# Kernel tuning notes

Hardware: AMD Instinct MI355X
Metric: run time of the kernel (lower is better)

The kernel has to match this reference:

```python
import jax, jax.numpy as jnp
import numpy as np

H = 4096
I = 11008
S = 4096
B = 1


def _swiglu_mlp(x, Wgu, Wd):
    # x: [B, T, H]; Wgu: [H, 2I]; Wd: [I, H]
    gu = jnp.einsum('bth,hi->bti', x, Wgu)
    gate, up = gu[..., :I], gu[..., I:]
    return jnp.einsum('bti,ih->bth', jax.nn.silu(gate) * up, Wd)


def setup_inputs() -> dict:
    key = jax.random.key(0)
    ks = jax.random.split(key, 5)
    scale_h = 1.0 / np.sqrt(H)
    scale_i = 1.0 / np.sqrt(I)
    hidden_states = jax.random.normal(ks[0], (B, S, H), dtype=jnp.float32)
    lang_ids = jnp.arange(S // 2, dtype=jnp.int64 if jax.config.jax_enable_x64 else jnp.int32)
    vision_ids = jnp.arange(S // 2, S, dtype=lang_ids.dtype)
    Wgu_lang = jax.random.normal(ks[1], (H, 2 * I), dtype=jnp.float32) * scale_h
    Wd_lang = jax.random.normal(ks[2], (I, H), dtype=jnp.float32) * scale_i
    Wgu_vis = jax.random.normal(ks[3], (H, 2 * I), dtype=jnp.float32) * scale_h
    Wd_vis = jax.random.normal(ks[4], (I, H), dtype=jnp.float32) * scale_i
    return {
        'hidden_states': hidden_states,
        'lang_ids': lang_ids,
        'vision_ids': vision_ids,
        'Wgu_lang': Wgu_lang,
        'Wd_lang': Wd_lang,
        'Wgu_vis': Wgu_vis,
        'Wd_vis': Wd_vis,
    }


def reference(hidden_states, lang_ids, vision_ids, Wgu_lang, Wd_lang, Wgu_vis, Wd_vis):
    # gather-by-token-type -> SwiGLU MLP per expert -> scatter-combine
    lang_out = _swiglu_mlp(hidden_states[:, lang_ids], Wgu_lang, Wd_lang)
    vis_out = _swiglu_mlp(hidden_states[:, vision_ids], Wgu_vis, Wd_vis)
    out = jnp.zeros_like(hidden_states)
    out = out.at[:, lang_ids].set(lang_out)
    out = out.at[:, vision_ids].set(vis_out)
    return out
```

## Files before the change

kernel.cpp:

```cpp
#include <hip/hip_runtime.h>
#include <hip/hip_bf16.h>


#define HDIM 4096
#define IDIM 11008
#define N2   22016
#define MTOK 2048
#define BM   128
#define BN   128
#define BK   64
#define KT1  64
#define KT2  172
#define NB1  86
#define NB2  32

typedef unsigned short ushort_t;
using f32x4  = __attribute__((ext_vector_type(4))) float;
using bf16x8 = __attribute__((ext_vector_type(8))) short;
using u32x2  = __attribute__((ext_vector_type(2))) unsigned int;
using u32x4  = __attribute__((ext_vector_type(4))) unsigned int;

__device__ __forceinline__ unsigned int bf16rne(float f) {
    unsigned int u = __builtin_bit_cast(unsigned int, f);
    return (u + 0x7FFFu + ((u >> 16) & 1u)) >> 16;
}
__device__ __forceinline__ unsigned int pack2(float lo, float hi) {
    return bf16rne(lo) | (bf16rne(hi) << 16);
}
__device__ __forceinline__ void gl_lds16(const void* g, void* l) {
    __builtin_amdgcn_global_load_lds(
        (const __attribute__((address_space(1))) void*)g,
        (__attribute__((address_space(3))) void*)l, 16, 0, 0);
}


__global__ __launch_bounds__(256)
void conv_x(const float* __restrict__ X, ushort_t* __restrict__ XP) {
    int bid = blockIdx.x;
    int rb = bid >> 6, kt = bid & 63;
    int t = threadIdx.x;
    int r0 = t >> 4, c4 = t & 15;
    ushort_t* tp = XP + (long)bid * 8192;
#pragma unroll
    for (int p = 0; p < 8; ++p) {
        int r = r0 + p * 16;
        f32x4 v = *(const f32x4*)(X + (long)(rb * 128 + r) * HDIM + kt * 64 + c4 * 4);
        u32x2 pk = { pack2(v[0], v[1]), pack2(v[2], v[3]) };
        int off = r * 64 + ((((c4 >> 1) ^ (r & 7)) << 3)) + ((c4 & 1) << 2);
        *(u32x2*)&tp[off] = pk;
    }
}

__device__ __forceinline__ void conv_w_tile(const float* W, ushort_t* tp, long ld,
                                            long krow0, long col0, int t) {
    int kp = t >> 5, c4 = t & 31;
    const float* p = W + (krow0 + kp * 8) * ld + col0 + c4 * 4;
    f32x4 v[8];
#pragma unroll
    for (int j = 0; j < 8; ++j) v[j] = *(const f32x4*)(p + (long)j * ld);
#pragma unroll
    for (int c = 0; c < 4; ++c) {
        int n = c4 * 4 + c;
        u32x4 pk = { pack2(v[0][c], v[1][c]), pack2(v[2][c], v[3][c]),
                     pack2(v[4][c], v[5][c]), pack2(v[6][c], v[7][c]) };
        int off = n * 64 + ((kp ^ (n & 7)) << 3);
        *(u32x4*)&tp[off] = pk;
    }
}

__global__ __launch_bounds__(256)
void conv_wgu(const float* __restrict__ W, ushort_t* __restrict__ WP) {
    int bid = blockIdx.x;
    int e = bid & 1, kt = (bid >> 1) & 63, nb = bid >> 7;
    conv_w_tile(W, WP + (long)bid * 8192, N2, (long)kt * 64,
                (long)e * IDIM + (long)nb * 128, threadIdx.x);
}

__global__ __launch_bounds__(256)
void conv_wd(const float* __restrict__ W, ushort_t* __restrict__ WP) {
    int bid = blockIdx.x;
    int kt = bid % KT2, nb = bid / KT2;
    conv_w_tile(W, WP + (long)bid * 8192, HDIM, (long)kt * 64,
                (long)nb * 128, threadIdx.x);
}

__global__ __launch_bounds__(256, 2)
void gu2_kernel(const ushort_t* __restrict__ XP, const ushort_t* __restrict__ WP,
                ushort_t* __restrict__ HP) {
    __shared__ ushort_t lds[24576];

    int nwg = gridDim.x;
    int cpx = nwg >> 3;
    int sw  = (blockIdx.x & 7) * cpx + (blockIdx.x >> 3);
    int mblk = sw & 15;
    int nblk = sw >> 4;

    const int t    = threadIdx.x;
    const int lane = t & 63;
    const int w    = t >> 6;
    const int wm   = w >> 1, wn = w & 1;
    const int rr   = lane & 15, g4 = lane >> 4;

    f32x4 accg[4][4] = {};
    f32x4 accu[4][4] = {};

    const ushort_t* srcA0 = XP + (long)(mblk * 64) * 8192;
    const ushort_t* srcG0 = WP + (long)(nblk * 64) * 2 * 8192;

    for (int kt = 0; kt < KT1; ++kt) {
        __syncthreads();
        const ushort_t* sA = srcA0 + (long)kt * 8192;
        const ushort_t* sG = srcG0 + (long)kt * 2 * 8192;
#pragma unroll
        for (int j = 0; j < 12; ++j) {
            int q = j * 4 + w;
            const ushort_t* s = (j < 4) ? sA : (j < 8) ? sG : (sG + 8192);
            gl_lds16(s + ((q & 15) << 9) + lane * 8, &lds[q << 9]);
        }
        __syncthreads();
#pragma unroll
        for (int ks = 0; ks < 2; ++ks) {
            const int c = ks * 4 + g4;
            bf16x8 a[4], bg[4], bu[4];
#pragma unroll
            for (int mf = 0; mf < 4; ++mf) {
                int r = wm * 64 + mf * 16 + rr;
                a[mf] = *(const bf16x8*)&lds[r * 64 + ((c ^ (r & 7)) << 3)];
            }
#pragma unroll
            for (int nf = 0; nf < 4; ++nf) {
                int r = wn * 64 + nf * 16 + rr;
                int off = r * 64 + ((c ^ (r & 7)) << 3);
                bg[nf] = *(const bf16x8*)&lds[8192 + off];
                bu[nf] = *(const bf16x8*)&lds[16384 + off];
            }
#pragma unroll
            for (int mf = 0; mf < 4; ++mf)
#pragma unroll
                for (int nf = 0; nf < 4; ++nf) {
                    accg[mf][nf] = __builtin_amdgcn_mfma_f32_16x16x32_bf16(a[mf], bg[nf], accg[mf][nf], 0, 0, 0);
                    accu[mf][nf] = __builtin_amdgcn_mfma_f32_16x16x32_bf16(a[mf], bu[nf], accu[mf][nf], 0, 0, 0);
                }
        }
    }
#pragma unroll
    for (int nf = 0; nf < 4; ++nf) {
        int nloc = wn * 64 + nf * 16 + rr;
        int kt2  = nblk * 2 + (nloc >> 6);
        int kk   = nloc & 63;
        ushort_t* tp = HP + (long)(mblk * KT2 + kt2) * 8192;
        int obase = ((kk >> 3) << 3) + (kk & 7);
#pragma unroll
        for (int mf = 0; mf < 4; ++mf)
#pragma unroll
            for (int i = 0; i < 4; ++i) {
                int r = wm * 64 + mf * 16 + g4 * 4 + i;
                float gv = accg[mf][nf][i];
                float uv = accu[mf][nf][i];
                float s  = gv / (1.0f + __expf(-gv));
                int off = r * 64 + ((((kk >> 3) ^ (r & 7)) << 3)) + (kk & 7);
                tp[off] = (ushort_t)bf16rne(s * uv);
            }
        (void)obase;
    }
}

__global__ __launch_bounds__(256, 3)
void down2_kernel(const ushort_t* __restrict__ HP, const ushort_t* __restrict__ WP,
                  float* __restrict__ Out) {
    __shared__ ushort_t lds[16384];

    int nwg = gridDim.x;
    int cpx = nwg >> 3;
    int sw  = (blockIdx.x & 7) * cpx + (blockIdx.x >> 3);
    int mblk = sw & 15;
    int nblk = sw >> 4;

    const int t    = threadIdx.x;
    const int lane = t & 63;
    const int w    = t >> 6;
    const int wm   = w >> 1, wn = w & 1;
    const int rr   = lane & 15, g4 = lane >> 4;

    f32x4 acc[4][4] = {};

    const ushort_t* srcA0 = HP + (long)(mblk * KT2) * 8192;
    const ushort_t* srcB0 = WP + (long)(nblk * KT2) * 8192;

    for (int kt = 0; kt < KT2; ++kt) {
        __syncthreads();
        const ushort_t* sA = srcA0 + (long)kt * 8192;
        const ushort_t* sB = srcB0 + (long)kt * 8192;
#pragma unroll
        for (int j = 0; j < 8; ++j) {
            int q = j * 4 + w;
            const ushort_t* s = (j < 4) ? sA : sB;
            gl_lds16(s + ((q & 15) << 9) + lane * 8, &lds[q << 9]);
        }
        __syncthreads();
#pragma unroll
        for (int ks = 0; ks < 2; ++ks) {
            const int c = ks * 4 + g4;
            bf16x8 a[4], b[4];
#pragma unroll
            for (int mf = 0; mf < 4; ++mf) {
                int r = wm * 64 + mf * 16 + rr;
                a[mf] = *(const bf16x8*)&lds[r * 64 + ((c ^ (r & 7)) << 3)];
            }
#pragma unroll
            for (int nf = 0; nf < 4; ++nf) {
                int r = wn * 64 + nf * 16 + rr;
                b[nf] = *(const bf16x8*)&lds[8192 + r * 64 + ((c ^ (r & 7)) << 3)];
            }
#pragma unroll
            for (int mf = 0; mf < 4; ++mf)
#pragma unroll
                for (int nf = 0; nf < 4; ++nf)
                    acc[mf][nf] = __builtin_amdgcn_mfma_f32_16x16x32_bf16(a[mf], b[nf], acc[mf][nf], 0, 0, 0);
        }
    }
#pragma unroll
    for (int mf = 0; mf < 4; ++mf)
#pragma unroll
        for (int nf = 0; nf < 4; ++nf)
#pragma unroll
            for (int i = 0; i < 4; ++i) {
                int m = mblk * 128 + wm * 64 + mf * 16 + g4 * 4 + i;
                int n = nblk * 128 + wn * 64 + nf * 16 + rr;
                Out[(long)m * HDIM + n] = acc[mf][nf][i];
            }
}

__device__ __forceinline__ int swz(int r) { return ((r >> 2) + ((r & 3) << 1)) & 7; }

__global__ __launch_bounds__(256, 2)
void gu_kernel(const float* __restrict__ X, const float* __restrict__ W,
               ushort_t* __restrict__ Hbuf) {
    __shared__ short As[BM * BK];
    __shared__ short Bg[BN * BK];
    __shared__ short Bu[BN * BK];
    int nwg = gridDim.x;
    int cpx = nwg >> 3;
    int sw  = (blockIdx.x & 7) * cpx + (blockIdx.x >> 3);
    int mblk = sw & 15, nblk = sw >> 4;
    const int m0 = mblk * BM, n0 = nblk * BN;
    const int t = threadIdx.x, lane = t & 63, w = t >> 6;
    const int wm = w >> 1, wn = w & 1, rr = lane & 15, g4 = lane >> 4;
    const int nc = t & 31, kc = t >> 5;
    f32x4 accg[4][4] = {}, accu[4][4] = {};
    for (int k0 = 0; k0 < HDIM; k0 += BK) {
        __syncthreads();
#pragma unroll
        for (int i = 0; i < 8; ++i) {
            int idx = t + i * 256, m = idx >> 4, c4 = idx & 15;
            f32x4 v = *(const f32x4*)(X + (long)(m0 + m) * HDIM + k0 + c4 * 4);
            u32x2 pk = { pack2(v[0], v[1]), pack2(v[2], v[3]) };
            *(u32x2*)&As[(m << 6) + ((((c4 >> 1) + swz(m)) & 7) << 3) + ((c4 & 1) << 2)] = pk;
        }
#pragma unroll
        for (int e = 0; e < 2; ++e) {
            const float* Wp = W + (long)(k0 + kc * 8) * N2 + (e ? (IDIM + n0) : n0) + nc * 4;
            short* Bl = e ? Bu : Bg;
#pragma unroll
            for (int h = 0; h < 2; ++h) {
                f32x4 r0 = *(const f32x4*)(Wp + (long)(h * 4 + 0) * N2);
                f32x4 r1 = *(const f32x4*)(Wp + (long)(h * 4 + 1) * N2);
                f32x4 r2 = *(const f32x4*)(Wp + (long)(h * 4 + 2) * N2);
                f32x4 r3 = *(const f32x4*)(Wp + (long)(h * 4 + 3) * N2);
#pragma unroll
                for (int c2 = 0; c2 < 4; ++c2) {
                    int n = nc * 4 + c2;
                    u32x2 pk = { pack2(r0[c2], r1[c2]), pack2(r2[c2], r3[c2]) };
                    *(u32x2*)&Bl[(n << 6) + (((kc + swz(n)) & 7) << 3) + (h << 2)] = pk;
                }
            }
        }
        __syncthreads();
#pragma unroll
        for (int ks = 0; ks < 2; ++ks) {
            bf16x8 a[4], bg[4], bu[4];
#pragma unroll
            for (int mf = 0; mf < 4; ++mf) {
                int r = wm * 64 + mf * 16 + rr;
                a[mf] = *(const bf16x8*)&As[(r << 6) + ((((ks * 4 + g4) + swz(r)) & 7) << 3)];
            }
#pragma unroll
            for (int nf = 0; nf < 4; ++nf) {
                int r = wn * 64 + nf * 16 + rr;
                int off = (r << 6) + ((((ks * 4 + g4) + swz(r)) & 7) << 3);
                bg[nf] = *(const bf16x8*)&Bg[off];
                bu[nf] = *(const bf16x8*)&Bu[off];
            }
#pragma unroll
            for (int mf = 0; mf < 4; ++mf)
#pragma unroll
                for (int nf = 0; nf < 4; ++nf) {
                    accg[mf][nf] = __builtin_amdgcn_mfma_f32_16x16x32_bf16(a[mf], bg[nf], accg[mf][nf], 0, 0, 0);
                    accu[mf][nf] = __builtin_amdgcn_mfma_f32_16x16x32_bf16(a[mf], bu[nf], accu[mf][nf], 0, 0, 0);
                }
        }
    }
#pragma unroll
    for (int mf = 0; mf < 4; ++mf)
#pragma unroll
        for (int nf = 0; nf < 4; ++nf)
#pragma unroll
            for (int i = 0; i < 4; ++i) {
                int m = m0 + wm * 64 + mf * 16 + g4 * 4 + i;
                int n = n0 + wn * 64 + nf * 16 + rr;
                float gv = accg[mf][nf][i], uv = accu[mf][nf][i];
                Hbuf[(long)m * IDIM + n] = (ushort_t)bf16rne(gv / (1.0f + __expf(-gv)) * uv);
            }
}

__global__ __launch_bounds__(256, 2)
void down_kernel(const ushort_t* __restrict__ Hbuf, const float* __restrict__ W,
                 float* __restrict__ Out) {
    __shared__ short As[BM * BK];
    __shared__ short Bs[BN * BK];
    int nwg = gridDim.x;
    int cpx = nwg >> 3;
    int sw  = (blockIdx.x & 7) * cpx + (blockIdx.x >> 3);
    int mblk = sw & 15, nblk = sw >> 4;
    const int m0 = mblk * BM, n0 = nblk * BN;
    const int t = threadIdx.x, lane = t & 63, w = t >> 6;
    const int wm = w >> 1, wn = w & 1, rr = lane & 15, g4 = lane >> 4;
    const int nc = t & 31, kc = t >> 5;
    f32x4 acc[4][4] = {};
    for (int k0 = 0; k0 < IDIM; k0 += BK) {
        __syncthreads();
#pragma unroll
        for (int i = 0; i < 4; ++i) {
            int idx = t + i * 256, m = idx >> 3, kc8 = idx & 7;
            u32x4 v = *(const u32x4*)(Hbuf + (long)(m0 + m) * IDIM + k0 + kc8 * 8);
            *(u32x4*)&As[(m << 6) + (((kc8 + swz(m)) & 7) << 3)] = v;
        }
        {
            const float* Wp = W + (long)(k0 + kc * 8) * HDIM + n0 + nc * 4;
#pragma unroll
            for (int h = 0; h < 2; ++h) {
                f32x4 r0 = *(const f32x4*)(Wp + (long)(h * 4 + 0) * HDIM);
                f32x4 r1 = *(const f32x4*)(Wp + (long)(h * 4 + 1) * HDIM);
                f32x4 r2 = *(const f32x4*)(Wp + (long)(h * 4 + 2) * HDIM);
                f32x4 r3 = *(const f32x4*)(Wp + (long)(h * 4 + 3) * HDIM);
#pragma unroll
                for (int c2 = 0; c2 < 4; ++c2) {
                    int n = nc * 4 + c2;
                    u32x2 pk = { pack2(r0[c2], r1[c2]), pack2(r2[c2], r3[c2]) };
                    *(u32x2*)&Bs[(n << 6) + (((kc + swz(n)) & 7) << 3) + (h << 2)] = pk;
                }
            }
        }
        __syncthreads();
#pragma unroll
        for (int ks = 0; ks < 2; ++ks) {
            bf16x8 a[4], b[4];
#pragma unroll
            for (int mf = 0; mf < 4; ++mf) {
                int r = wm * 64 + mf * 16 + rr;
                a[mf] = *(const bf16x8*)&As[(r << 6) + ((((ks * 4 + g4) + swz(r)) & 7) << 3)];
            }
#pragma unroll
            for (int nf = 0; nf < 4; ++nf) {
                int r = wn * 64 + nf * 16 + rr;
                b[nf] = *(const bf16x8*)&Bs[(r << 6) + ((((ks * 4 + g4) + swz(r)) & 7) << 3)];
            }
#pragma unroll
            for (int mf = 0; mf < 4; ++mf)
#pragma unroll
                for (int nf = 0; nf < 4; ++nf)
                    acc[mf][nf] = __builtin_amdgcn_mfma_f32_16x16x32_bf16(a[mf], b[nf], acc[mf][nf], 0, 0, 0);
        }
    }
#pragma unroll
    for (int mf = 0; mf < 4; ++mf)
#pragma unroll
        for (int nf = 0; nf < 4; ++nf)
#pragma unroll
            for (int i = 0; i < 4; ++i) {
                int m = m0 + wm * 64 + mf * 16 + g4 * 4 + i;
                int n = n0 + wn * 64 + nf * 16 + rr;
                Out[(long)m * HDIM + n] = acc[mf][nf][i];
            }
}

extern "C" void kernel_launch(void* const* d_in, const int* in_sizes, int n_in,
                              void* d_out, int out_size, void* d_ws, size_t ws_size,
                              hipStream_t stream) {
    const float* x     = (const float*)d_in[0];
    const float* Wgu_l = (const float*)d_in[3];
    const float* Wd_l  = (const float*)d_in[4];
    const float* Wgu_v = (const float*)d_in[5];
    const float* Wd_v  = (const float*)d_in[6];
    float* out         = (float*)d_out;

    const size_t XP_B = (size_t)16 * KT1 * 16384;
    const size_t HP_B = (size_t)16 * KT2 * 16384;
    const size_t WP_B = (size_t)NB1 * KT1 * 2 * 16384;
    const size_t NEED = XP_B + HP_B + WP_B;

    if (ws_size >= NEED) {
        ushort_t* XP = (ushort_t*)d_ws;
        ushort_t* HP = XP + XP_B / 2;
        ushort_t* WP = HP + HP_B / 2;
        for (int e = 0; e < 2; ++e) {
            const float* xe = x + (long)e * MTOK * HDIM;
            float*       oe = out + (long)e * MTOK * HDIM;
            conv_x  <<<dim3(16 * KT1),      dim3(256), 0, stream>>>(xe, XP);
            conv_wgu<<<dim3(NB1 * KT1 * 2), dim3(256), 0, stream>>>(e ? Wgu_v : Wgu_l, WP);
            gu2_kernel<<<dim3(16 * NB1),    dim3(256), 0, stream>>>(XP, WP, HP);
            conv_wd <<<dim3(NB2 * KT2),     dim3(256), 0, stream>>>(e ? Wd_v : Wd_l, WP);
            down2_kernel<<<dim3(16 * NB2),  dim3(256), 0, stream>>>(HP, WP, oe);
        }
    } else {
        ushort_t* hbuf = (ushort_t*)d_ws;
        for (int e = 0; e < 2; ++e) {
            const float* Wgu = e ? Wgu_v : Wgu_l;
            const float* Wd  = e ? Wd_v  : Wd_l;
            const float* xe  = x   + (long)e * MTOK * HDIM;
            float*       oe  = out + (long)e * MTOK * HDIM;
            gu_kernel  <<<dim3(16 * NB1), dim3(256), 0, stream>>>(xe, Wgu, hbuf);
            down_kernel<<<dim3(16 * NB2), dim3(256), 0, stream>>>(hbuf, Wd, oe);
        }
    }
}
```

Before: 1.469 ms.

## Double-buffer LDS with 256-row tiles and 8 waves in both GEMM kernels

```diff
diff --git a/kernel.cpp b/kernel.cpp
--- a/kernel.cpp
+++ b/kernel.cpp
@@ -37,34 +37,19 @@
 __global__ __launch_bounds__(256)
 void conv_x(const float* __restrict__ X, ushort_t* __restrict__ XP) {
     int bid = blockIdx.x;
-    int rb = bid >> 6, kt = bid & 63;
+    int mb = bid >> 6, kt = bid & 63;
     int t = threadIdx.x;
     int r0 = t >> 4, c4 = t & 15;
-    ushort_t* tp = XP + (long)bid * 8192;
+    int kh = c4 >> 3, c = (c4 >> 1) & 3, lo4 = (c4 & 1) << 2;
+    ushort_t* tp = XP + ((long)(mb >> 1) * KT1 + kt) * 16384 + (long)kh * 8192 + (mb & 1) * 4096;
 #pragma unroll
     for (int p = 0; p < 8; ++p) {
-        int r = r0 + p * 16;
-        f32x4 v = *(const f32x4*)(X + (long)(rb * 128 + r) * HDIM + kt * 64 + c4 * 4);
+        int rl = r0 + p * 16;
+        f32x4 v = *(const f32x4*)(X + (long)(mb * 128 + rl) * HDIM + kt * 64 + c4 * 4);
         u32x2 pk = { pack2(v[0], v[1]), pack2(v[2], v[3]) };
-        int off = r * 64 + ((((c4 >> 1) ^ (r & 7)) << 3)) + ((c4 & 1) << 2);
-        *(u32x2*)&tp[off] = pk;
-    }
-}
-
-__device__ __forceinline__ void conv_w_tile(const float* W, ushort_t* tp, long ld,
-                                            long krow0, long col0, int t) {
-    int kp = t >> 5, c4 = t & 31;
-    const float* p = W + (krow0 + kp * 8) * ld + col0 + c4 * 4;
-    f32x4 v[8];
-#pragma unroll
-    for (int j = 0; j < 8; ++j) v[j] = *(const f32x4*)(p + (long)j * ld);
-#pragma unroll
-    for (int c = 0; c < 4; ++c) {
-        int n = c4 * 4 + c;
-        u32x4 pk = { pack2(v[0][c], v[1][c]), pack2(v[2][c], v[3][c]),
-                     pack2(v[4][c], v[5][c]), pack2(v[6][c], v[7][c]) };
-        int off = n * 64 + ((kp ^ (n & 7)) << 3);
-        *(u32x4*)&tp[off] = pk;
+        int q = rl >> 1;
+        int pos = ((((rl & 1) << 2) | c) ^ (q & 7));
+        *(u32x2*)&tp[q * 64 + pos * 8 + lo4] = pk;
     }
 }
 
@@ -72,161 +57,255 @@
 void conv_wgu(const float* __restrict__ W, ushort_t* __restrict__ WP) {
     int bid = blockIdx.x;
     int e = bid & 1, kt = (bid >> 1) & 63, nb = bid >> 7;
-    conv_w_tile(W, WP + (long)bid * 8192, N2, (long)kt * 64,
-                (long)e * IDIM + (long)nb * 128, threadIdx.x);
+    int t = threadIdx.x;
+    int kp = t >> 5, c4 = t & 31;
+    const float* p = W + ((long)kt * 64 + kp * 8) * N2 + (long)e * IDIM + nb * 128 + c4 * 4;
+    f32x4 v[8];
+#pragma unroll
+    for (int j = 0; j < 8; ++j) v[j] = *(const f32x4*)(p + (long)j * N2);
+    ushort_t* tp = WP + ((long)nb * KT1 + kt) * 16384 + (long)(kp >> 2) * 8192 + e * 4096;
+    int c = kp & 3;
+#pragma unroll
+    for (int cc = 0; cc < 4; ++cc) {
+        int n = c4 * 4 + cc;
+        int q = n >> 1;
+        int pos = ((((n & 1) << 2) | c) ^ (q & 7));
+        u32x4 pk = { pack2(v[0][cc], v[1][cc]), pack2(v[2][cc], v[3][cc]),
+                     pack2(v[4][cc], v[5][cc]), pack2(v[6][cc], v[7][cc]) };
+        *(u32x4*)&tp[q * 64 + pos * 8] = pk;
+    }
 }
 
 __global__ __launch_bounds__(256)
 void conv_wd(const float* __restrict__ W, ushort_t* __restrict__ WP) {
     int bid = blockIdx.x;
     int kt = bid % KT2, nb = bid / KT2;
-    conv_w_tile(W, WP + (long)bid * 8192, HDIM, (long)kt * 64,
-                (long)nb * 128, threadIdx.x);
-}
-
-__global__ __launch_bounds__(256, 2)
-void gu2_kernel(const ushort_t* __restrict__ XP, const ushort_t* __restrict__ WP,
+    int t = threadIdx.x;
+    int kp = t >> 5, c4 = t & 31;
+    const float* p = W + ((long)kt * 64 + kp * 8) * HDIM + nb * 128 + c4 * 4;
+    f32x4 v[8];
+#pragma unroll
+    for (int j = 0; j < 8; ++j) v[j] = *(const f32x4*)(p + (long)j * HDIM);
+    ushort_t* tp = WP + ((long)nb * KT2 + kt) * 8192 + (long)(kp >> 2) * 4096;
+    int c = kp & 3;
+#pragma unroll
+    for (int cc = 0; cc < 4; ++cc) {
+        int n = c4 * 4 + cc;
+        int q = n >> 1;
+        int pos = ((((n & 1) << 2) | c) ^ (q & 7));
+        u32x4 pk = { pack2(v[0][cc], v[1][cc]), pack2(v[2][cc], v[3][cc]),
+                     pack2(v[4][cc], v[5][cc]), pack2(v[6][cc], v[7][cc]) };
+        *(u32x4*)&tp[q * 64 + pos * 8] = pk;
+    }
+}
+
+#define STAGE_U(SRC, DSTOFF) do { \
+    gl_lds16((SRC) + so + lane * 8, &lds[(DSTOFF) + so]); \
+    gl_lds16((SRC) + 4096 + so + lane * 8, &lds[(DSTOFF) + 4096 + so]); } while (0)
+
+#define MFMA16(ACC, AF, BF) \
+    _Pragma("unroll") \
+    for (int mf = 0; mf < 4; ++mf) \
+        _Pragma("unroll") \
+        for (int nf = 0; nf < 4; ++nf) \
+            ACC[mf][nf] = __builtin_amdgcn_mfma_f32_16x16x32_bf16(AF[mf], BF[nf], ACC[mf][nf], 0, 0, 0);
+
+#define VMCNT_MID(N) do { \
+    if (pf) asm volatile("s_waitcnt vmcnt(" #N ")" ::: "memory"); \
+    else    asm volatile("s_waitcnt vmcnt(0)" ::: "memory"); } while (0)
+#define VMCNT_END(N) do { \
+    if (pf) asm volatile("s_waitcnt vmcnt(" #N ")" ::: "memory"); } while (0)
+
+__global__ __launch_bounds__(512, 2)
+void gu3_kernel(const ushort_t* __restrict__ XP, const ushort_t* __restrict__ WP,
                 ushort_t* __restrict__ HP) {
-    __shared__ ushort_t lds[24576];
-
+    __shared__ ushort_t lds[65536];
     int nwg = gridDim.x;
     int cpx = nwg >> 3;
     int sw  = (blockIdx.x & 7) * cpx + (blockIdx.x >> 3);
-    int mblk = sw & 15;
-    int nblk = sw >> 4;
-
-    const int t    = threadIdx.x;
-    const int lane = t & 63;
-    const int w    = t >> 6;
-    const int wm   = w >> 1, wn = w & 1;
-    const int rr   = lane & 15, g4 = lane >> 4;
-
-    f32x4 accg[4][4] = {};
-    f32x4 accu[4][4] = {};
-
-    const ushort_t* srcA0 = XP + (long)(mblk * 64) * 8192;
-    const ushort_t* srcG0 = WP + (long)(nblk * 64) * 2 * 8192;
-
+    int mblk = sw & 7;
+    int nblk = sw >> 3;
+    const int t = threadIdx.x, lane = t & 63, w = t >> 6;
+    const int wr = w >> 1, wc = w & 1;
+    const int rr = lane & 15, g4 = lane >> 4;
+    const int so = w * 512;
+
+    int aoff[4], boff[4];
+#pragma unroll
+    for (int mf = 0; mf < 4; ++mf) {
+        int m = wr * 64 + mf * 16 + rr, q = m >> 1;
+        aoff[mf] = q * 64 + ((((((m & 1) << 2) | g4) ^ (q & 7))) << 3);
+    }
+#pragma unroll
+    for (int nf = 0; nf < 4; ++nf) {
+        int n = wc * 64 + nf * 16 + rr, q = n >> 1;
+        boff[nf] = q * 64 + ((((((n & 1) << 2) | g4) ^ (q & 7))) << 3);
+    }
+
+    f32x4 accg[4][4] = {}, accu[4][4] = {};
+    const ushort_t* srcA = XP + (long)mblk * KT1 * 16384;
+    const ushort_t* srcB = WP + (long)nblk * KT1 * 16384;
+
+    STAGE_U(srcA, 0);
+    STAGE_U(srcB, 8192);
+    STAGE_U(srcA + 8192, 16384);
+    STAGE_U(srcB + 8192, 24576);
+    asm volatile("s_waitcnt vmcnt(0)" ::: "memory");
+    __builtin_amdgcn_s_barrier();
+
+    int cur = 0;
     for (int kt = 0; kt < KT1; ++kt) {
-        __syncthreads();
-        const ushort_t* sA = srcA0 + (long)kt * 8192;
-        const ushort_t* sG = srcG0 + (long)kt * 2 * 8192;
-#pragma unroll
-        for (int j = 0; j < 12; ++j) {
-            int q = j * 4 + w;
-            const ushort_t* s = (j < 4) ? sA : (j < 8) ? sG : (sG + 8192);
-            gl_lds16(s + ((q & 15) << 9) + lane * 8, &lds[q << 9]);
-        }
-        __syncthreads();
-#pragma unroll
-        for (int ks = 0; ks < 2; ++ks) {
-            const int c = ks * 4 + g4;
-            bf16x8 a[4], bg[4], bu[4];
-#pragma unroll
-            for (int mf = 0; mf < 4; ++mf) {
-                int r = wm * 64 + mf * 16 + rr;
-                a[mf] = *(const bf16x8*)&lds[r * 64 + ((c ^ (r & 7)) << 3)];
-            }
-#pragma unroll
-            for (int nf = 0; nf < 4; ++nf) {
-                int r = wn * 64 + nf * 16 + rr;
-                int off = r * 64 + ((c ^ (r & 7)) << 3);
-                bg[nf] = *(const bf16x8*)&lds[8192 + off];
-                bu[nf] = *(const bf16x8*)&lds[16384 + off];
-            }
-#pragma unroll
-            for (int mf = 0; mf < 4; ++mf)
-#pragma unroll
-                for (int nf = 0; nf < 4; ++nf) {
-                    accg[mf][nf] = __builtin_amdgcn_mfma_f32_16x16x32_bf16(a[mf], bg[nf], accg[mf][nf], 0, 0, 0);
-                    accu[mf][nf] = __builtin_amdgcn_mfma_f32_16x16x32_bf16(a[mf], bu[nf], accu[mf][nf], 0, 0, 0);
-                }
-        }
-    }
+        const int cb = cur * 32768, pb = (cur ^ 1) * 32768;
+        const ushort_t* nA = srcA + (long)(kt + 1) * 16384;
+        const ushort_t* nB = srcB + (long)(kt + 1) * 16384;
+        const bool pf = (kt + 1 < KT1);
+        bf16x8 af[4], bfr[4];
+
+#pragma unroll
+        for (int mf = 0; mf < 4; ++mf) af[mf] = *(const bf16x8*)&lds[cb + aoff[mf]];
+#pragma unroll
+        for (int nf = 0; nf < 4; ++nf) bfr[nf] = *(const bf16x8*)&lds[cb + 8192 + boff[nf]];
+        if (pf) STAGE_U(nA, pb);
+        __builtin_amdgcn_s_barrier();
+        __builtin_amdgcn_s_setprio(1);
+        MFMA16(accg, af, bfr);
+        __builtin_amdgcn_s_setprio(0);
+        __builtin_amdgcn_s_barrier();
+
+#pragma unroll
+        for (int nf = 0; nf < 4; ++nf) bfr[nf] = *(const bf16x8*)&lds[cb + 12288 + boff[nf]];
+        if (pf) STAGE_U(nB, pb + 8192);
+        __builtin_amdgcn_s_barrier();
+        __builtin_amdgcn_s_setprio(1);
+        MFMA16(accu, af, bfr);
+        __builtin_amdgcn_s_setprio(0);
+        VMCNT_MID(4);
+        __builtin_amdgcn_s_barrier();
+
+#pragma unroll
+        for (int mf = 0; mf < 4; ++mf) af[mf] = *(const bf16x8*)&lds[cb + 16384 + aoff[mf]];
+#pragma unroll
+        for (int nf = 0; nf < 4; ++nf) bfr[nf] = *(const bf16x8*)&lds[cb + 24576 + boff[nf]];
+        if (pf) STAGE_U(nA + 8192, pb + 16384);
+        __builtin_amdgcn_s_barrier();
+        __builtin_amdgcn_s_setprio(1);
+        MFMA16(accg, af, bfr);
+        __builtin_amdgcn_s_setprio(0);
+        __builtin_amdgcn_s_barrier();
+
+#pragma unroll
+        for (int nf = 0; nf < 4; ++nf) bfr[nf] = *(const bf16x8*)&lds[cb + 28672 + boff[nf]];
+        if (pf) STAGE_U(nB + 8192, pb + 24576);
+        __builtin_amdgcn_s_barrier();
+        __builtin_amdgcn_s_setprio(1);
+        MFMA16(accu, af, bfr);
+        __builtin_amdgcn_s_setprio(0);
+        VMCNT_END(4);
+        __builtin_amdgcn_s_barrier();
+
+        cur ^= 1;
+    }
+
 #pragma unroll
     for (int nf = 0; nf < 4; ++nf) {
-        int nloc = wn * 64 + nf * 16 + rr;
-        int kt2  = nblk * 2 + (nloc >> 6);
-        int kk   = nloc & 63;
-        ushort_t* tp = HP + (long)(mblk * KT2 + kt2) * 8192;
-        int obase = ((kk >> 3) << 3) + (kk & 7);
+        int nloc = wc * 64 + nf * 16 + rr;
+        int kt2 = nblk * 2 + (nloc >> 6);
+        int k = nloc & 63;
+        int kh = k >> 5, c = (k >> 3) & 3, klow = k & 7;
+        ushort_t* tp = HP + ((long)mblk * KT2 + kt2) * 16384 + kh * 8192 + klow;
 #pragma unroll
         for (int mf = 0; mf < 4; ++mf)
 #pragma unroll
             for (int i = 0; i < 4; ++i) {
-                int r = wm * 64 + mf * 16 + g4 * 4 + i;
-                float gv = accg[mf][nf][i];
-                float uv = accu[mf][nf][i];
-                float s  = gv / (1.0f + __expf(-gv));
-                int off = r * 64 + ((((kk >> 3) ^ (r & 7)) << 3)) + (kk & 7);
-                tp[off] = (ushort_t)bf16rne(s * uv);
-            }
-        (void)obase;
-    }
-}
-
-__global__ __launch_bounds__(256, 3)
-void down2_kernel(const ushort_t* __restrict__ HP, const ushort_t* __restrict__ WP,
+                int m = wr * 64 + mf * 16 + g4 * 4 + i;
+                int q = m >> 1;
+                int pos = ((((m & 1) << 2) | c) ^ (q & 7));
+                float gv = accg[mf][nf][i], uv = accu[mf][nf][i];
+                float s = gv / (1.0f + __expf(-gv));
+                tp[q * 64 + pos * 8] = (ushort_t)bf16rne(s * uv);
+            }
+    }
+}
+
+__global__ __launch_bounds__(512, 2)
+void down3_kernel(const ushort_t* __restrict__ HP, const ushort_t* __restrict__ WP,
                   float* __restrict__ Out) {
-    __shared__ ushort_t lds[16384];
-
+    __shared__ ushort_t lds[49152];
     int nwg = gridDim.x;
     int cpx = nwg >> 3;
     int sw  = (blockIdx.x & 7) * cpx + (blockIdx.x >> 3);
-    int mblk = sw & 15;
-    int nblk = sw >> 4;
-
-    const int t    = threadIdx.x;
-    const int lane = t & 63;
-    const int w    = t >> 6;
-    const int wm   = w >> 1, wn = w & 1;
-    const int rr   = lane & 15, g4 = lane >> 4;
+    int mblk = sw & 7;
+    int nblk = sw >> 3;
+    const int t = threadIdx.x, lane = t & 63, w = t >> 6;
+    const int wr = w >> 1, wc = w & 1;
+    const int rr = lane & 15, g4 = lane >> 4;
+    const int so = w * 512;
+
+    int aoff[4], boff[4];
+#pragma unroll
+    for (int mf = 0; mf < 4; ++mf) {
+        int m = wr * 64 + mf * 16 + rr, q = m >> 1;
+        aoff[mf] = q * 64 + ((((((m & 1) << 2) | g4) ^ (q & 7))) << 3);
+    }
+#pragma unroll
+    for (int nf = 0; nf < 4; ++nf) {
+        int n = wc * 64 + nf * 16 + rr, q = n >> 1;
+        boff[nf] = q * 64 + ((((((n & 1) << 2) | g4) ^ (q & 7))) << 3);
+    }
 
     f32x4 acc[4][4] = {};
-
-    const ushort_t* srcA0 = HP + (long)(mblk * KT2) * 8192;
-    const ushort_t* srcB0 = WP + (long)(nblk * KT2) * 8192;
-
+    const ushort_t* srcA = HP + (long)mblk * KT2 * 16384;
+    const ushort_t* srcB = WP + (long)nblk * KT2 * 8192;
+
+    STAGE_U(srcA, 0);
+    STAGE_U(srcA + 8192, 8192);
+    STAGE_U(srcB, 16384);
+    asm volatile("s_waitcnt vmcnt(0)" ::: "memory");
+    __builtin_amdgcn_s_barrier();
+
+    int cur = 0;
     for (int kt = 0; kt < KT2; ++kt) {
-        __syncthreads();
-        const ushort_t* sA = srcA0 + (long)kt * 8192;
-        const ushort_t* sB = srcB0 + (long)kt * 8192;
-#pragma unroll
-        for (int j = 0; j < 8; ++j) {
-            int q = j * 4 + w;
-            const ushort_t* s = (j < 4) ? sA : sB;
-            gl_lds16(s + ((q & 15) << 9) + lane * 8, &lds[q << 9]);
-        }
-        __syncthreads();
-#pragma unroll
-        for (int ks = 0; ks < 2; ++ks) {
-            const int c = ks * 4 + g4;
-            bf16x8 a[4], b[4];
-#pragma unroll
-            for (int mf = 0; mf < 4; ++mf) {
-                int r = wm * 64 + mf * 16 + rr;
-                a[mf] = *(const bf16x8*)&lds[r * 64 + ((c ^ (r & 7)) << 3)];
-            }
-#pragma unroll
-            for (int nf = 0; nf < 4; ++nf) {
-                int r = wn * 64 + nf * 16 + rr;
-                b[nf] = *(const bf16x8*)&lds[8192 + r * 64 + ((c ^ (r & 7)) << 3)];
-            }
-#pragma unroll
-            for (int mf = 0; mf < 4; ++mf)
-#pragma unroll
-                for (int nf = 0; nf < 4; ++nf)
-                    acc[mf][nf] = __builtin_amdgcn_mfma_f32_16x16x32_bf16(a[mf], b[nf], acc[mf][nf], 0, 0, 0);
-        }
-    }
+        const int cb = cur * 24576, pb = (cur ^ 1) * 24576;
+        const ushort_t* nA = srcA + (long)(kt + 1) * 16384;
+        const ushort_t* nB = srcB + (long)(kt + 1) * 8192;
+        const bool pf = (kt + 1 < KT2);
+        bf16x8 af[4], bfr[4];
+
+#pragma unroll
+        for (int mf = 0; mf < 4; ++mf) af[mf] = *(const bf16x8*)&lds[cb + aoff[mf]];
+#pragma unroll
+        for (int nf = 0; nf < 4; ++nf) bfr[nf] = *(const bf16x8*)&lds[cb + 16384 + boff[nf]];
+        if (pf) { STAGE_U(nA, pb); STAGE_U(nB, pb + 16384); }
+        __builtin_amdgcn_s_barrier();
+        __builtin_amdgcn_s_setprio(1);
+        MFMA16(acc, af, bfr);
+        __builtin_amdgcn_s_setprio(0);
+        VMCNT_MID(4);
+        __builtin_amdgcn_s_barrier();
+
+#pragma unroll
+        for (int mf = 0; mf < 4; ++mf) af[mf] = *(const bf16x8*)&lds[cb + 8192 + aoff[mf]];
+#pragma unroll
+        for (int nf = 0; nf < 4; ++nf) bfr[nf] = *(const bf16x8*)&lds[cb + 20480 + boff[nf]];
+        if (pf) STAGE_U(nA + 8192, pb + 8192);
+        __builtin_amdgcn_s_barrier();
+        __builtin_amdgcn_s_setprio(1);
+        MFMA16(acc, af, bfr);
+        __builtin_amdgcn_s_setprio(0);
+        VMCNT_END(2);
+        __builtin_amdgcn_s_barrier();
+
+        cur ^= 1;
+    }
+
 #pragma unroll
     for (int mf = 0; mf < 4; ++mf)
 #pragma unroll
         for (int nf = 0; nf < 4; ++nf)
 #pragma unroll
             for (int i = 0; i < 4; ++i) {
-                int m = mblk * 128 + wm * 64 + mf * 16 + g4 * 4 + i;
-                int n = nblk * 128 + wn * 64 + nf * 16 + rr;
+                int m = mblk * 256 + wr * 64 + mf * 16 + g4 * 4 + i;
+                int n = nblk * 128 + wc * 64 + nf * 16 + rr;
                 Out[(long)m * HDIM + n] = acc[mf][nf][i];
             }
 }
@@ -394,9 +473,9 @@
     const float* Wd_v  = (const float*)d_in[6];
     float* out         = (float*)d_out;
 
-    const size_t XP_B = (size_t)16 * KT1 * 16384;
-    const size_t HP_B = (size_t)16 * KT2 * 16384;
-    const size_t WP_B = (size_t)NB1 * KT1 * 2 * 16384;
+    const size_t XP_B = (size_t)8 * KT1 * 32768;
+    const size_t HP_B = (size_t)8 * KT2 * 32768;
+    const size_t WP_B = (size_t)NB1 * KT1 * 32768;
     const size_t NEED = XP_B + HP_B + WP_B;
 
     if (ws_size >= NEED) {
@@ -408,9 +487,9 @@
             float*       oe = out + (long)e * MTOK * HDIM;
             conv_x  <<<dim3(16 * KT1),      dim3(256), 0, stream>>>(xe, XP);
             conv_wgu<<<dim3(NB1 * KT1 * 2), dim3(256), 0, stream>>>(e ? Wgu_v : Wgu_l, WP);
-            gu2_kernel<<<dim3(16 * NB1),    dim3(256), 0, stream>>>(XP, WP, HP);
+            gu3_kernel<<<dim3(8 * NB1),     dim3(512), 0, stream>>>(XP, WP, HP);
             conv_wd <<<dim3(NB2 * KT2),     dim3(256), 0, stream>>>(e ? Wd_v : Wd_l, WP);
-            down2_kernel<<<dim3(16 * NB2),  dim3(256), 0, stream>>>(HP, WP, oe);
+            down3_kernel<<<dim3(8 * NB2),   dim3(512), 0, stream>>>(HP, WP, oe);
         }
     } else {
         ushort_t* hbuf = (ushort_t*)d_ws;
```

After: 1.308 ms. 1.12x faster.
